# Kernel optimization log

Hardware: AMD Instinct MI355X
Metric: run time of the kernel (lower is better)

## Reference

```python
import jax, jax.numpy as jnp
import numpy as np

N = 100000   # nodes
E = 1600000  # edges
C = 64       # hidden_channels
EPS = 1e-7   # module eps
BN_EPS = 1e-5


def setup_inputs() -> dict:
    key = jax.random.key(0)
    ks = jax.random.split(key, 6)
    x = jax.random.normal(ks[0], (N, C), jnp.float32)
    edge_index = jax.random.randint(ks[1], (2, E), 0, N)
    W1 = jax.random.normal(ks[2], (2, C, 2 * C), jnp.float32) * 0.1
    b1 = jnp.zeros((2, 2 * C), jnp.float32)
    g1 = jnp.ones((2, 2 * C), jnp.float32)
    be1 = jnp.zeros((2, 2 * C), jnp.float32)
    W2 = jax.random.normal(ks[3], (2, 2 * C, C), jnp.float32) * 0.1
    b2 = jnp.zeros((2, C), jnp.float32)
    t = jnp.ones((2,), jnp.float32)       # SoftmaxAggregation learnable temperature
    scale = jnp.ones((2,), jnp.float32)   # MessageNorm learnable scale
    bn_g = jnp.ones((2, C), jnp.float32)
    bn_b = jnp.zeros((2, C), jnp.float32)
    return dict(x=x, edge_index=edge_index, t=t, scale=scale, W1=W1, b1=b1,
                g1=g1, be1=be1, W2=W2, b2=b2, bn_g=bn_g, bn_b=bn_b)


def _batchnorm(h, g, b):
    # training-mode BatchNorm1d: biased batch statistics
    mu = h.mean(axis=0)
    var = h.var(axis=0)
    return (h - mu) * jax.lax.rsqrt(var + BN_EPS) * g + b


def _gga_conv(x, src, dst, t, scale, W1, b1, g1, be1, W2, b2):
    # message: relu(x_j) + eps  (gather over source nodes)
    msg = jax.nn.relu(x[src]) + EPS                     # [E, C]
    # segment-wise (per dst node) softmax over edges, per channel
    logits = msg * t
    m = jax.ops.segment_max(logits, dst, num_segments=N)  # [N, C]
    e = jnp.exp(logits - m[dst])
    denom = jax.ops.segment_sum(e, dst, num_segments=N)   # [N, C]
    alpha = e / denom[dst]
    agg = jax.ops.segment_sum(msg * alpha, dst, num_segments=N)  # [N, C]
    # MessageNorm(learn_scale=True): x + scale * ||x|| * normalize(agg)
    msg_n = agg / jnp.maximum(jnp.linalg.norm(agg, axis=-1, keepdims=True), 1e-12)
    x_norm = jnp.linalg.norm(x, axis=-1, keepdims=True)
    out = x + msg_n * x_norm * scale
    # MLP [C, 2C, C]: Linear -> BatchNorm -> ReLU -> Linear (plain last)
    h = jax.nn.relu(_batchnorm(out @ W1 + b1, g1, be1))
    return h @ W2 + b2


def reference(x, edge_index, t, scale, W1, b1, g1, be1, W2, b2, bn_g, bn_b):
    src, dst = edge_index[0], edge_index[1]
    intter = x
    for i in range(2):  # block_size = 2
        x = _gga_conv(x, src, dst, t[i], scale[i], W1[i], b1[i], g1[i],
                      be1[i], W2[i], b2[i])
        x = _batchnorm(x, bn_g[i], bn_b[i])
        if i < 1:
            x = jax.nn.relu(x) + EPS
    # residual + relu + eps; dropout p=0 is identity
    return jax.nn.relu(intter + x) + EPS
```

## Files before the change

kernel.cpp:

```cpp
#include <hip/hip_runtime.h>
#include <hip/hip_bf16.h>

#define C 64
#define H 128
#define FEPS 1e-7f
#define BNE 1e-5f
#define BSH 9
#define BSZ 512
#define EPB 4096

typedef __attribute__((ext_vector_type(8))) short bf16x8;
typedef __attribute__((ext_vector_type(4))) float f32x4;

__device__ __forceinline__ float us2f(ushort u) {
    unsigned int x = ((unsigned int)u) << 16;
    return __uint_as_float(x);
}
__device__ __forceinline__ ushort f2us(float f) {
    __hip_bfloat16 h = __float2bfloat16(f);
    return *reinterpret_cast<ushort*>(&h);
}

__global__ __launch_bounds__(256) void bhist_k(const int* __restrict__ dst,
                                               int* __restrict__ bucket_cnt, int E, int NB) {
    __shared__ int cnt[256];
    int tid = threadIdx.x;
    cnt[tid] = 0;
    __syncthreads();
    int base = blockIdx.x * EPB;
#pragma unroll
    for (int j = 0; j < 16; j++) {
        int e = base + tid + j * 256;
        if (e < E) atomicAdd(&cnt[dst[e] >> BSH], 1);
    }
    __syncthreads();
    if (tid < NB && cnt[tid]) atomicAdd(&bucket_cnt[tid], cnt[tid]);
}

__global__ void bscan_k(const int* __restrict__ bucket_cnt, int* __restrict__ bucket_off,
                        int* __restrict__ bucket_fill, int* __restrict__ row_start,
                        int NB, int N, int E) {
    __shared__ int s[256];
    int tid = threadIdx.x;
    int v = (tid < NB) ? bucket_cnt[tid] : 0;
    s[tid] = v;
    __syncthreads();
    for (int off = 1; off < 256; off <<= 1) {
        int t = 0;
        if (tid >= off) t = s[tid - off];
        __syncthreads();
        s[tid] += t;
        __syncthreads();
    }
    int excl = s[tid] - v;
    if (tid < NB) { bucket_off[tid] = excl; bucket_fill[tid] = excl; }
    if (tid == NB - 1) bucket_off[NB] = s[tid];
    if (tid == 0) row_start[N] = E;
}

__global__ __launch_bounds__(256) void bscat_k(const int* __restrict__ src,
                                               const int* __restrict__ dst,
                                               int* __restrict__ bucket_fill,
                                               unsigned int* __restrict__ bpak, int E) {
    __shared__ int cnt[256];
    __shared__ int sbase[256];
    int tid = threadIdx.x;
    cnt[tid] = 0;
    __syncthreads();
    int base = blockIdx.x * EPB;
    int dd[16], rk[16];
#pragma unroll
    for (int j = 0; j < 16; j++) {
        int e = base + tid + j * 256;
        dd[j] = -1;
        if (e < E) {
            int d = dst[e];
            dd[j] = d;
            rk[j] = atomicAdd(&cnt[d >> BSH], 1);
        }
    }
    __syncthreads();
    if (cnt[tid]) sbase[tid] = atomicAdd(&bucket_fill[tid], cnt[tid]);
    __syncthreads();
#pragma unroll
    for (int j = 0; j < 16; j++) {
        if (dd[j] >= 0) {
            int e = base + tid + j * 256;
            int b = dd[j] >> BSH;
            int pos = sbase[b] + rk[j];
            bpak[pos] = ((unsigned int)(dd[j] & (BSZ - 1)) << 17) | (unsigned int)src[e];
        }
    }
}

__global__ __launch_bounds__(512) void bfine_k(const int* __restrict__ bucket_off,
                                               const unsigned int* __restrict__ bpak,
                                               int* __restrict__ row_start,
                                               int* __restrict__ col, int N) {
    __shared__ int cnt[BSZ];
    __shared__ int off[BSZ];
    __shared__ int fill[BSZ];
    int tid = threadIdx.x;
    int b = blockIdx.x;
    int e0 = bucket_off[b], e1 = bucket_off[b + 1];
    int nbase = b << BSH;
    cnt[tid] = 0; fill[tid] = 0;
    __syncthreads();
    for (int e = e0 + tid; e < e1; e += 512) atomicAdd(&cnt[bpak[e] >> 17], 1);
    __syncthreads();
    int v = cnt[tid];
    off[tid] = v;
    __syncthreads();
    for (int o = 1; o < 512; o <<= 1) {
        int t = 0;
        if (tid >= o) t = off[tid - o];
        __syncthreads();
        off[tid] += t;
        __syncthreads();
    }
    int excl = off[tid] - v;
    off[tid] = excl;
    __syncthreads();
    int n = nbase + tid;
    if (n < N) row_start[n] = e0 + excl;
    for (int e = e0 + tid; e < e1; e += 512) {
        unsigned int w = bpak[e];
        int loc = w >> 17;
        int r = atomicAdd(&fill[loc], 1);
        col[e0 + off[loc] + r] = (int)(w & 0x1FFFFu);
    }
}

__global__ __launch_bounds__(256) void dhist_k(const int* __restrict__ rs,
                                               int* __restrict__ dbin, int N) {
    __shared__ int h[64];
    int tid = threadIdx.x;
    if (tid < 64) h[tid] = 0;
    __syncthreads();
#pragma unroll
    for (int j = 0; j < 4; j++) {
        int i = blockIdx.x * 1024 + tid + j * 256;
        if (i < N) {
            int deg = rs[i + 1] - rs[i];
            atomicAdd(&h[min(deg, 63)], 1);
        }
    }
    __syncthreads();
    if (tid < 64 && h[tid]) atomicAdd(&dbin[tid], h[tid]);
}

__global__ void dscan_k(const int* __restrict__ dbin, int* __restrict__ dbfill) {
    __shared__ int s[64];
    int tid = threadIdx.x;
    int v = dbin[tid];
    s[tid] = v;
    __syncthreads();
    for (int o = 1; o < 64; o <<= 1) {
        int t = 0;
        if (tid >= o) t = s[tid - o];
        __syncthreads();
        s[tid] += t;
        __syncthreads();
    }
    dbfill[tid] = s[tid] - v;
}

__global__ __launch_bounds__(256) void dscat_k(const int* __restrict__ rs,
                                               int* __restrict__ dbfill,
                                               int* __restrict__ perm, int N) {
    __shared__ int cnt[64];
    __shared__ int sb[64];
    int tid = threadIdx.x;
    if (tid < 64) cnt[tid] = 0;
    __syncthreads();
    int bn[4], rk[4];
#pragma unroll
    for (int j = 0; j < 4; j++) {
        int i = blockIdx.x * 1024 + tid + j * 256;
        bn[j] = -1;
        if (i < N) {
            int deg = rs[i + 1] - rs[i];
            bn[j] = min(deg, 63);
            rk[j] = atomicAdd(&cnt[bn[j]], 1);
        }
    }
    __syncthreads();
    if (tid < 64 && cnt[tid]) sb[tid] = atomicAdd(&dbfill[tid], cnt[tid]);
    __syncthreads();
#pragma unroll
    for (int j = 0; j < 4; j++) {
        if (bn[j] >= 0) {
            int i = blockIdx.x * 1024 + tid + j * 256;
            perm[sb[bn[j]] + rk[j]] = i;
        }
    }
}

template <int AFF>
__global__ __launch_bounds__(256) void prep_k(const float* __restrict__ in,
                                              const float* __restrict__ fa,
                                              const float* __restrict__ fc,
                                              ushort* __restrict__ marr, int total4) {
    int i = blockIdx.x * 256 + threadIdx.x;
    if (i >= total4) return;
    float4 v = ((const float4*)in)[i];
    int c0 = (i * 4) & 63;
    float vv[4] = {v.x, v.y, v.z, v.w};
    ushort u[4];
#pragma unroll
    for (int j = 0; j < 4; j++) {
        float x = vv[j];
        if (AFF) {
            float xv = fmaxf(x * fa[c0 + j] + fc[c0 + j], 0.f) + FEPS;
            x = xv + FEPS;
        } else {
            x = fmaxf(x, 0.f) + FEPS;
        }
        u[j] = f2us(x);
    }
    ushort4 uv = make_ushort4(u[0], u[1], u[2], u[3]);
    ((ushort4*)marr)[i] = uv;
}

template <int MODE>
__global__ __launch_bounds__(256) void agg_k(const float* __restrict__ xin,
                                             const float* __restrict__ ta,
                                             const float* __restrict__ tc,
                                             const uint2* __restrict__ marr64,
                                             const int* __restrict__ rs,
                                             const int* __restrict__ col,
                                             const int* __restrict__ perm,
                                             const float* __restrict__ t,
                                             const float* __restrict__ sc,
                                             int layer, float* __restrict__ outb, int N) {
    int lane = threadIdx.x & 63;
    int wid = threadIdx.x >> 6;
    int q = lane >> 4;
    int ql = lane & 15;
    int gid = blockIdx.x * 16 + wid * 4 + q;
    if (gid >= N) return;
    int n = perm[gid];
    float tv = t[layer];
    float sv = sc[layer];

    int beg = rs[n], end = rs[n + 1];
    float den[4] = {0.f, 0.f, 0.f, 0.f}, num[4] = {0.f, 0.f, 0.f, 0.f};

    auto acc4 = [&](uint2 d) {
        float m0 = __uint_as_float(d.x << 16);
        float m1 = __uint_as_float(d.x & 0xffff0000u);
        float m2 = __uint_as_float(d.y << 16);
        float m3 = __uint_as_float(d.y & 0xffff0000u);
        float e0 = __expf(m0 * tv);
        float e1 = __expf(m1 * tv);
        float e2 = __expf(m2 * tv);
        float e3 = __expf(m3 * tv);
        den[0] += e0; num[0] += m0 * e0;
        den[1] += e1; num[1] += m1 * e1;
        den[2] += e2; num[2] += m2 * e2;
        den[3] += e3; num[3] += m3 * e3;
    };

    int e = beg;
    int head = (4 - (e & 3)) & 3;
    if (head > end - e) head = end - e;
    for (int i = 0; i < head; i++, e++) {
        uint2 d0 = marr64[(size_t)col[e] * 16 + ql];
        acc4(d0);
    }
    if (e + 8 <= end) {
        int4 ca = *(const int4*)(col + e);
        int4 cb = *(const int4*)(col + e + 4);
        while (true) {
            uint2 d0 = marr64[(size_t)ca.x * 16 + ql];
            uint2 d1 = marr64[(size_t)ca.y * 16 + ql];
            uint2 d2 = marr64[(size_t)ca.z * 16 + ql];
            uint2 d3 = marr64[(size_t)ca.w * 16 + ql];
            uint2 d4 = marr64[(size_t)cb.x * 16 + ql];
            uint2 d5 = marr64[(size_t)cb.y * 16 + ql];
            uint2 d6 = marr64[(size_t)cb.z * 16 + ql];
            uint2 d7 = marr64[(size_t)cb.w * 16 + ql];
            e += 8;
            bool more = (e + 8 <= end);
            if (more) {
                ca = *(const int4*)(col + e);
                cb = *(const int4*)(col + e + 4);
            }
            acc4(d0); acc4(d1); acc4(d2); acc4(d3);
            acc4(d4); acc4(d5); acc4(d6); acc4(d7);
            if (!more) break;
        }
    }
    for (; e < end; e++) {
        uint2 d0 = marr64[(size_t)col[e] * 16 + ql];
        acc4(d0);
    }

    float agg[4], aq = 0.f;
#pragma unroll
    for (int c = 0; c < 4; c++) {
        agg[c] = (den[c] > 0.f) ? (num[c] / den[c]) : 0.f;
        aq += agg[c] * agg[c];
    }

    float4 xv = ((const float4*)xin)[(size_t)n * 16 + ql];
    float xn[4];
    if (MODE == 0) {
        xn[0] = xv.x; xn[1] = xv.y; xn[2] = xv.z; xn[3] = xv.w;
    } else {
        float4 av = ((const float4*)ta)[ql];
        float4 cv = ((const float4*)tc)[ql];
        xn[0] = fmaxf(xv.x * av.x + cv.x, 0.f) + FEPS;
        xn[1] = fmaxf(xv.y * av.y + cv.y, 0.f) + FEPS;
        xn[2] = fmaxf(xv.z * av.z + cv.z, 0.f) + FEPS;
        xn[3] = fmaxf(xv.w * av.w + cv.w, 0.f) + FEPS;
    }
    float xq = xn[0] * xn[0] + xn[1] * xn[1] + xn[2] * xn[2] + xn[3] * xn[3];
    float na = aq, nx = xq;
#pragma unroll
    for (int m = 1; m <= 8; m <<= 1) {
        na += __shfl_xor(na, m, 64);
        nx += __shfl_xor(nx, m, 64);
    }
    float s = (1.0f / fmaxf(sqrtf(na), 1e-12f)) * sqrtf(nx) * sv;
    float4 o;
    o.x = xn[0] + agg[0] * s;
    o.y = xn[1] + agg[1] * s;
    o.z = xn[2] + agg[2] * s;
    o.w = xn[3] + agg[3] * s;
    ((float4*)outb)[(size_t)n * 16 + ql] = o;
}

__global__ void wprep_k(const float* __restrict__ W1, const float* __restrict__ W2,
                        ushort* __restrict__ wt1, ushort* __restrict__ wt2) {
    int idx = blockIdx.x * 256 + threadIdx.x;
    int m = idx >> 13, w = idx & 8191;
    if (m < 2) {
        int colw = w >> 6, k = w & 63;
        wt1[idx] = f2us(W1[m * 8192 + k * 128 + colw]);
    } else {
        int l = m - 2;
        int colw = w >> 7, k = w & 127;
        wt2[l * 8192 + w] = f2us(W2[l * 8192 + k * 64 + colw]);
    }
}

template <int KD, int ND, int MODE>
__global__ __launch_bounds__(256) void mlpm_k(const void* __restrict__ Ain,
                                              const float* __restrict__ fa,
                                              const float* __restrict__ fc,
                                              const ushort* __restrict__ WtT,
                                              const float* __restrict__ bias,
                                              void* __restrict__ outp,
                                              float* __restrict__ s_sum,
                                              float* __restrict__ s_ssq, int N) {
    constexpr int NT = ND / 16;
    constexpr int KS = KD / 32;
    __shared__ float ssum[ND], sssq[ND];
    int tid = threadIdx.x;
    int wave = tid >> 6, lane = tid & 63, lrow = lane & 15, kg = lane >> 4;
    if (tid < ND) { ssum[tid] = 0.f; sssq[tid] = 0.f; }
    __syncthreads();

    int base = blockIdx.x * 128;

    bf16x8 wfr[NT][KS];
#pragma unroll
    for (int t = 0; t < NT; t++)
#pragma unroll
        for (int ks = 0; ks < KS; ks++)
            wfr[t][ks] = *(const bf16x8*)(WtT + (t * 16 + lrow) * KD + ks * 32 + kg * 8);
    float bv[NT];
#pragma unroll
    for (int t = 0; t < NT; t++) bv[t] = bias[t * 16 + lrow];

    float ls[NT], lq[NT];
#pragma unroll
    for (int t = 0; t < NT; t++) { ls[t] = 0.f; lq[t] = 0.f; }

    bf16x8 afr[2][KS];
    if (MODE == 0) {
        float4 raw[2][KS][2];
#pragma unroll
        for (int rt = 0; rt < 2; rt++) {
            int arow = base + (wave * 2 + rt) * 16 + lrow;
            bool rok = arow < N;
#pragma unroll
            for (int ks = 0; ks < KS; ks++) {
                float4 z = make_float4(0.f, 0.f, 0.f, 0.f);
                raw[rt][ks][0] = z; raw[rt][ks][1] = z;
                if (rok) {
                    const float4* p = (const float4*)((const float*)Ain +
                                                      (size_t)arow * KD + ks * 32 + kg * 8);
                    raw[rt][ks][0] = p[0];
                    raw[rt][ks][1] = p[1];
                }
            }
        }
#pragma unroll
        for (int rt = 0; rt < 2; rt++)
#pragma unroll
            for (int ks = 0; ks < KS; ks++) {
                float4 v0 = raw[rt][ks][0], v1 = raw[rt][ks][1];
                bf16x8 a;
                a[0] = (short)f2us(v0.x); a[1] = (short)f2us(v0.y);
                a[2] = (short)f2us(v0.z); a[3] = (short)f2us(v0.w);
                a[4] = (short)f2us(v1.x); a[5] = (short)f2us(v1.y);
                a[6] = (short)f2us(v1.z); a[7] = (short)f2us(v1.w);
                afr[rt][ks] = a;
            }
    } else {
        uint4 raw[2][KS];
#pragma unroll
        for (int rt = 0; rt < 2; rt++) {
            int arow = base + (wave * 2 + rt) * 16 + lrow;
            bool rok = arow < N;
#pragma unroll
            for (int ks = 0; ks < KS; ks++) {
                raw[rt][ks] = make_uint4(0u, 0u, 0u, 0u);
                if (rok) raw[rt][ks] = *(const uint4*)((const ushort*)Ain +
                                                       (size_t)arow * KD + ks * 32 + kg * 8);
            }
        }
#pragma unroll
        for (int rt = 0; rt < 2; rt++)
#pragma unroll
            for (int ks = 0; ks < KS; ks++) {
                int k0 = ks * 32 + kg * 8;
                float4 a0 = *(const float4*)(fa + k0);
                float4 a1 = *(const float4*)(fa + k0 + 4);
                float4 c0 = *(const float4*)(fc + k0);
                float4 c1 = *(const float4*)(fc + k0 + 4);
                unsigned int w[4] = {raw[rt][ks].x, raw[rt][ks].y, raw[rt][ks].z, raw[rt][ks].w};
                float av[8] = {a0.x, a0.y, a0.z, a0.w, a1.x, a1.y, a1.z, a1.w};
                float cv[8] = {c0.x, c0.y, c0.z, c0.w, c1.x, c1.y, c1.z, c1.w};
                bf16x8 a;
#pragma unroll
                for (int p = 0; p < 4; p++) {
                    float f0 = us2f((ushort)(w[p] & 0xffffu));
                    float f1 = us2f((ushort)(w[p] >> 16));
                    f0 = fmaxf(f0 * av[2 * p] + cv[2 * p], 0.f);
                    f1 = fmaxf(f1 * av[2 * p + 1] + cv[2 * p + 1], 0.f);
                    a[2 * p] = (short)f2us(f0);
                    a[2 * p + 1] = (short)f2us(f1);
                }
                afr[rt][ks] = a;
            }
    }

#pragma unroll
    for (int rt = 0; rt < 2; rt++) {
        int tidx = wave * 2 + rt;
#pragma unroll
        for (int t = 0; t < NT; t++) {
            f32x4 acc = {0.f, 0.f, 0.f, 0.f};
#pragma unroll
            for (int ks = 0; ks < KS; ks++)
                acc = __builtin_amdgcn_mfma_f32_16x16x32_bf16(afr[rt][ks], wfr[t][ks], acc, 0, 0, 0);
            int colw = t * 16 + lrow;
#pragma unroll
            for (int r = 0; r < 4; r++) {
                int orow = base + tidx * 16 + kg * 4 + r;
                float v = acc[r] + bv[t];
                if (orow < N) {
                    if (MODE == 0) ((ushort*)outp)[(size_t)orow * ND + colw] = f2us(v);
                    else ((float*)outp)[(size_t)orow * ND + colw] = v;
                    ls[t] += v; lq[t] += v * v;
                }
            }
        }
    }

#pragma unroll
    for (int t = 0; t < NT; t++) {
        float a = ls[t], b = lq[t];
        a += __shfl_xor(a, 16, 64); a += __shfl_xor(a, 32, 64);
        b += __shfl_xor(b, 16, 64); b += __shfl_xor(b, 32, 64);
        if (kg == 0) {
            atomicAdd(&ssum[t * 16 + lrow], a);
            atomicAdd(&sssq[t * 16 + lrow], b);
        }
    }
    __syncthreads();
    if (tid < ND) {
        atomicAdd(&s_sum[tid], ssum[tid]);
        atomicAdd(&s_ssq[tid], sssq[tid]);
    }
}

__global__ void bnfin_k(const float* __restrict__ sum, const float* __restrict__ ssq,
                        const float* __restrict__ g, const float* __restrict__ b,
                        float* __restrict__ a, float* __restrict__ cc, int n, float invN) {
    int i = threadIdx.x;
    if (i < n) {
        float mu = sum[i] * invN;
        float var = ssq[i] * invN - mu * mu;
        float rs = rsqrtf(var + BNE);
        float gg = g[i];
        float bb = b[i];
        a[i] = rs * gg;
        cc[i] = bb - mu * rs * gg;
    }
}

__global__ void final_k(const float4* __restrict__ x0, const float4* __restrict__ y,
                        const float* __restrict__ a2, const float* __restrict__ c2,
                        float4* __restrict__ outp, int total4) {
    int i = blockIdx.x * 256 + threadIdx.x;
    if (i >= total4) return;
    int c0 = (i * 4) & 63;
    float4 yv = y[i], xv = x0[i];
    float4 o;
    o.x = fmaxf(xv.x + yv.x * a2[c0 + 0] + c2[c0 + 0], 0.f) + FEPS;
    o.y = fmaxf(xv.y + yv.y * a2[c0 + 1] + c2[c0 + 1], 0.f) + FEPS;
    o.z = fmaxf(xv.z + yv.z * a2[c0 + 2] + c2[c0 + 2], 0.f) + FEPS;
    o.w = fmaxf(xv.w + yv.w * a2[c0 + 3] + c2[c0 + 3], 0.f) + FEPS;
    outp[i] = o;
}

extern "C" void kernel_launch(void* const* d_in, const int* in_sizes, int n_in,
                              void* d_out, int out_size, void* d_ws, size_t ws_size,
                              hipStream_t stream) {
    const float* x0 = (const float*)d_in[0];
    const int* ei = (const int*)d_in[1];
    const float* t = (const float*)d_in[2];
    const float* scale = (const float*)d_in[3];
    const float* W1 = (const float*)d_in[4];
    const float* b1 = (const float*)d_in[5];
    const float* g1 = (const float*)d_in[6];
    const float* be1 = (const float*)d_in[7];
    const float* W2 = (const float*)d_in[8];
    const float* b2 = (const float*)d_in[9];
    const float* bn_g = (const float*)d_in[10];
    const float* bn_b = (const float*)d_in[11];

    const int N = in_sizes[0] / C;
    const int E = in_sizes[1] / 2;
    const int* src = ei;
    const int* dst = ei + E;
    const int NB = (N + BSZ - 1) >> BSH;

    char* ws = (char*)d_ws;
    size_t cur = 0;
    auto alloc = [&](size_t bytes) -> char* {
        char* p = ws + cur;
        cur = (cur + bytes + 255) & ~(size_t)255;
        return p;
    };
    int* bucket_cnt = (int*)alloc(256 * 4);
    float* stats = (float*)alloc(768 * 4);
    int* dbin = (int*)alloc(64 * 4);
    size_t zbytes = cur;
    float* params = (float*)alloc(768 * 4);
    int* bucket_off = (int*)alloc(257 * 4);
    int* bucket_fill = (int*)alloc(256 * 4);
    int* dbfill = (int*)alloc(64 * 4);
    int* perm = (int*)alloc((size_t)N * 4);
    int* row_start = (int*)alloc(((size_t)N + 1) * 4);
    int* col = (int*)alloc((size_t)E * 4);
    ushort* marr = (ushort*)alloc((size_t)N * C * 2);
    ushort* wt1 = (ushort*)alloc(2 * H * C * 2);
    ushort* wt2 = (ushort*)alloc(2 * C * H * 2);
    float* bout = (float*)alloc((size_t)N * C * 4);
    ushort* bh = (ushort*)alloc((size_t)N * H * 2);
    float* by = (float*)alloc((size_t)N * C * 4);
    unsigned int* bpak = (unsigned int*)bh;

    hipMemsetAsync(d_ws, 0, zbytes, stream);

    wprep_k<<<128, 256, 0, stream>>>(W1, W2, wt1, wt2);

    int nbE = (E + EPB - 1) / EPB;
    bhist_k<<<nbE, 256, 0, stream>>>(dst, bucket_cnt, E, NB);
    bscan_k<<<1, 256, 0, stream>>>(bucket_cnt, bucket_off, bucket_fill, row_start, NB, N, E);
    bscat_k<<<nbE, 256, 0, stream>>>(src, dst, bucket_fill, bpak, E);
    bfine_k<<<NB, 512, 0, stream>>>(bucket_off, bpak, row_start, col, N);

    int nbD = (N + 1023) / 1024;
    dhist_k<<<nbD, 256, 0, stream>>>(row_start, dbin, N);
    dscan_k<<<1, 64, 0, stream>>>(dbin, dbfill);
    dscat_k<<<nbD, 256, 0, stream>>>(row_start, dbfill, perm, N);

    float* sum1_0 = stats + 0;   float* ssq1_0 = stats + 128;
    float* sum2_0 = stats + 256; float* ssq2_0 = stats + 320;
    float* sum1_1 = stats + 384; float* ssq1_1 = stats + 512;
    float* sum2_1 = stats + 640; float* ssq2_1 = stats + 704;
    float* a1_0 = params + 0;   float* c1_0 = params + 128;
    float* a2_0 = params + 256; float* c2_0 = params + 320;
    float* a1_1 = params + 384; float* c1_1 = params + 512;
    float* a2_1 = params + 640; float* c2_1 = params + 704;

    const float invN = 1.0f / (float)N;
    int nbN16 = (N + 15) / 16;
    int nbT2 = (N + 127) / 128;
    int nbP = (N * C / 4 + 255) / 256;

    prep_k<0><<<nbP, 256, 0, stream>>>(x0, nullptr, nullptr, marr, N * C / 4);
    agg_k<0><<<nbN16, 256, 0, stream>>>(x0, nullptr, nullptr,
                                        (const uint2*)marr, row_start, col, perm,
                                        t, scale, 0, bout, N);
    mlpm_k<C, H, 0><<<nbT2, 256, 0, stream>>>(bout, nullptr, nullptr, wt1, b1, bh,
                                              sum1_0, ssq1_0, N);
    bnfin_k<<<1, 128, 0, stream>>>(sum1_0, ssq1_0, g1, be1, a1_0, c1_0, H, invN);
    mlpm_k<H, C, 1><<<nbT2, 256, 0, stream>>>(bh, a1_0, c1_0, wt2, b2, by,
                                              sum2_0, ssq2_0, N);
    bnfin_k<<<1, 64, 0, stream>>>(sum2_0, ssq2_0, bn_g, bn_b, a2_0, c2_0, C, invN);

    prep_k<1><<<nbP, 256, 0, stream>>>(by, a2_0, c2_0, marr, N * C / 4);
    agg_k<1><<<nbN16, 256, 0, stream>>>(by, a2_0, c2_0,
                                        (const uint2*)marr, row_start, col, perm,
                                        t, scale, 1, bout, N);
    mlpm_k<C, H, 0><<<nbT2, 256, 0, stream>>>(bout, nullptr, nullptr, wt1 + H * C, b1 + H, bh,
                                              sum1_1, ssq1_1, N);
    bnfin_k<<<1, 128, 0, stream>>>(sum1_1, ssq1_1, g1 + H, be1 + H, a1_1, c1_1, H, invN);
    mlpm_k<H, C, 1><<<nbT2, 256, 0, stream>>>(bh, a1_1, c1_1, wt2 + C * H, b2 + C, by,
                                              sum2_1, ssq2_1, N);
    bnfin_k<<<1, 64, 0, stream>>>(sum2_1, ssq2_1, bn_g + C, bn_b + C, a2_1, c2_1, C, invN);

    final_k<<<nbP, 256, 0, stream>>>((const float4*)x0, (const float4*)by, a2_1, c2_1,
                                     (float4*)d_out, N * C / 4);
}
```

Before: 345.9 us.

## Fold BN finalize into consumers and drop degree-sorted node permutation

```diff
diff --git a/kernel.cpp b/kernel.cpp
--- a/kernel.cpp
+++ b/kernel.cpp
@@ -19,6 +19,17 @@
 __device__ __forceinline__ ushort f2us(float f) {
     __hip_bfloat16 h = __float2bfloat16(f);
     return *reinterpret_cast<ushort*>(&h);
+}
+__device__ __forceinline__ void bnaff(const float* __restrict__ sum,
+                                      const float* __restrict__ ssq,
+                                      const float* __restrict__ g,
+                                      const float* __restrict__ b,
+                                      float invN, int ch, float& a, float& c) {
+    float mu = sum[ch] * invN;
+    float var = ssq[ch] * invN - mu * mu;
+    float rs = rsqrtf(var + BNE);
+    a = rs * g[ch];
+    c = b[ch] - mu * a;
 }
 
 __global__ __launch_bounds__(256) void bhist_k(const int* __restrict__ dst,
@@ -131,75 +142,13 @@
     }
 }
 
-__global__ __launch_bounds__(256) void dhist_k(const int* __restrict__ rs,
-                                               int* __restrict__ dbin, int N) {
-    __shared__ int h[64];
-    int tid = threadIdx.x;
-    if (tid < 64) h[tid] = 0;
-    __syncthreads();
-#pragma unroll
-    for (int j = 0; j < 4; j++) {
-        int i = blockIdx.x * 1024 + tid + j * 256;
-        if (i < N) {
-            int deg = rs[i + 1] - rs[i];
-            atomicAdd(&h[min(deg, 63)], 1);
-        }
-    }
-    __syncthreads();
-    if (tid < 64 && h[tid]) atomicAdd(&dbin[tid], h[tid]);
-}
-
-__global__ void dscan_k(const int* __restrict__ dbin, int* __restrict__ dbfill) {
-    __shared__ int s[64];
-    int tid = threadIdx.x;
-    int v = dbin[tid];
-    s[tid] = v;
-    __syncthreads();
-    for (int o = 1; o < 64; o <<= 1) {
-        int t = 0;
-        if (tid >= o) t = s[tid - o];
-        __syncthreads();
-        s[tid] += t;
-        __syncthreads();
-    }
-    dbfill[tid] = s[tid] - v;
-}
-
-__global__ __launch_bounds__(256) void dscat_k(const int* __restrict__ rs,
-                                               int* __restrict__ dbfill,
-                                               int* __restrict__ perm, int N) {
-    __shared__ int cnt[64];
-    __shared__ int sb[64];
-    int tid = threadIdx.x;
-    if (tid < 64) cnt[tid] = 0;
-    __syncthreads();
-    int bn[4], rk[4];
-#pragma unroll
-    for (int j = 0; j < 4; j++) {
-        int i = blockIdx.x * 1024 + tid + j * 256;
-        bn[j] = -1;
-        if (i < N) {
-            int deg = rs[i + 1] - rs[i];
-            bn[j] = min(deg, 63);
-            rk[j] = atomicAdd(&cnt[bn[j]], 1);
-        }
-    }
-    __syncthreads();
-    if (tid < 64 && cnt[tid]) sb[tid] = atomicAdd(&dbfill[tid], cnt[tid]);
-    __syncthreads();
-#pragma unroll
-    for (int j = 0; j < 4; j++) {
-        if (bn[j] >= 0) {
-            int i = blockIdx.x * 1024 + tid + j * 256;
-            perm[sb[bn[j]] + rk[j]] = i;
-        }
-    }
-}
-
 template <int AFF>
 __global__ __launch_bounds__(256) void prep_k(const float* __restrict__ in,
-                                              const float* __restrict__ fa,
-                                              const float* __restrict__ fc,
+                                              const float* __restrict__ sum,
+                                              const float* __restrict__ ssq,
+                                              const float* __restrict__ g,
+                                              const float* __restrict__ b,
+                                              float invN,
                                               ushort* __restrict__ marr, int total4) {
     int i = blockIdx.x * 256 + threadIdx.x;
     if (i >= total4) return;
@@ -211,7 +160,9 @@
     for (int j = 0; j < 4; j++) {
         float x = vv[j];
         if (AFF) {
-            float xv = fmaxf(x * fa[c0 + j] + fc[c0 + j], 0.f) + FEPS;
+            float a, cc;
+            bnaff(sum, ssq, g, b, invN, c0 + j, a, cc);
+            float xv = fmaxf(x * a + cc, 0.f) + FEPS;
             x = xv + FEPS;
         } else {
             x = fmaxf(x, 0.f) + FEPS;
@@ -224,12 +175,14 @@
 
 template <int MODE>
 __global__ __launch_bounds__(256) void agg_k(const float* __restrict__ xin,
-                                             const float* __restrict__ ta,
-                                             const float* __restrict__ tc,
+                                             const float* __restrict__ sum,
+                                             const float* __restrict__ ssq,
+                                             const float* __restrict__ g,
+                                             const float* __restrict__ b,
+                                             float invN,
                                              const uint2* __restrict__ marr64,
                                              const int* __restrict__ rs,
                                              const int* __restrict__ col,
-                                             const int* __restrict__ perm,
                                              const float* __restrict__ t,
                                              const float* __restrict__ sc,
                                              int layer, float* __restrict__ outb, int N) {
@@ -237,9 +190,8 @@
     int wid = threadIdx.x >> 6;
     int q = lane >> 4;
     int ql = lane & 15;
-    int gid = blockIdx.x * 16 + wid * 4 + q;
-    if (gid >= N) return;
-    int n = perm[gid];
+    int n = blockIdx.x * 16 + wid * 4 + q;
+    if (n >= N) return;
     float tv = t[layer];
     float sv = sc[layer];
 
@@ -308,12 +260,13 @@
     if (MODE == 0) {
         xn[0] = xv.x; xn[1] = xv.y; xn[2] = xv.z; xn[3] = xv.w;
     } else {
-        float4 av = ((const float4*)ta)[ql];
-        float4 cv = ((const float4*)tc)[ql];
-        xn[0] = fmaxf(xv.x * av.x + cv.x, 0.f) + FEPS;
-        xn[1] = fmaxf(xv.y * av.y + cv.y, 0.f) + FEPS;
-        xn[2] = fmaxf(xv.z * av.z + cv.z, 0.f) + FEPS;
-        xn[3] = fmaxf(xv.w * av.w + cv.w, 0.f) + FEPS;
+        float vv[4] = {xv.x, xv.y, xv.z, xv.w};
+#pragma unroll
+        for (int j = 0; j < 4; j++) {
+            float a, cc;
+            bnaff(sum, ssq, g, b, invN, 4 * ql + j, a, cc);
+            xn[j] = fmaxf(vv[j] * a + cc, 0.f) + FEPS;
+        }
     }
     float xq = xn[0] * xn[0] + xn[1] * xn[1] + xn[2] * xn[2] + xn[3] * xn[3];
     float na = aq, nx = xq;
@@ -347,8 +300,11 @@
 
 template <int KD, int ND, int MODE>
 __global__ __launch_bounds__(256) void mlpm_k(const void* __restrict__ Ain,
-                                              const float* __restrict__ fa,
-                                              const float* __restrict__ fc,
+                                              const float* __restrict__ sum,
+                                              const float* __restrict__ ssq,
+                                              const float* __restrict__ g,
+                                              const float* __restrict__ b,
+                                              float invN,
                                               const ushort* __restrict__ WtT,
                                               const float* __restrict__ bias,
                                               void* __restrict__ outp,
@@ -357,9 +313,17 @@
     constexpr int NT = ND / 16;
     constexpr int KS = KD / 32;
     __shared__ float ssum[ND], sssq[ND];
+    __shared__ float faf[MODE ? KD : 1][2];
     int tid = threadIdx.x;
     int wave = tid >> 6, lane = tid & 63, lrow = lane & 15, kg = lane >> 4;
     if (tid < ND) { ssum[tid] = 0.f; sssq[tid] = 0.f; }
+    if (MODE) {
+        for (int i = tid; i < KD; i += 256) {
+            float a, cc;
+            bnaff(sum, ssq, g, b, invN, i, a, cc);
+            faf[i][0] = a; faf[i][1] = cc;
+        }
+    }
     __syncthreads();
 
     int base = blockIdx.x * 128;
@@ -427,20 +391,14 @@
 #pragma unroll
             for (int ks = 0; ks < KS; ks++) {
                 int k0 = ks * 32 + kg * 8;
-                float4 a0 = *(const float4*)(fa + k0);
-                float4 a1 = *(const float4*)(fa + k0 + 4);
-                float4 c0 = *(const float4*)(fc + k0);
-                float4 c1 = *(const float4*)(fc + k0 + 4);
                 unsigned int w[4] = {raw[rt][ks].x, raw[rt][ks].y, raw[rt][ks].z, raw[rt][ks].w};
-                float av[8] = {a0.x, a0.y, a0.z, a0.w, a1.x, a1.y, a1.z, a1.w};
-                float cv[8] = {c0.x, c0.y, c0.z, c0.w, c1.x, c1.y, c1.z, c1.w};
                 bf16x8 a;
 #pragma unroll
                 for (int p = 0; p < 4; p++) {
                     float f0 = us2f((ushort)(w[p] & 0xffffu));
                     float f1 = us2f((ushort)(w[p] >> 16));
-                    f0 = fmaxf(f0 * av[2 * p] + cv[2 * p], 0.f);
-                    f1 = fmaxf(f1 * av[2 * p + 1] + cv[2 * p + 1], 0.f);
+                    f0 = fmaxf(f0 * faf[k0 + 2 * p][0] + faf[k0 + 2 * p][1], 0.f);
+                    f1 = fmaxf(f1 * faf[k0 + 2 * p + 1][0] + faf[k0 + 2 * p + 1][1], 0.f);
                     a[2 * p] = (short)f2us(f0);
                     a[2 * p + 1] = (short)f2us(f1);
                 }
@@ -473,12 +431,12 @@
 
 #pragma unroll
     for (int t = 0; t < NT; t++) {
-        float a = ls[t], b = lq[t];
+        float a = ls[t], bq = lq[t];
         a += __shfl_xor(a, 16, 64); a += __shfl_xor(a, 32, 64);
-        b += __shfl_xor(b, 16, 64); b += __shfl_xor(b, 32, 64);
+        bq += __shfl_xor(bq, 16, 64); bq += __shfl_xor(bq, 32, 64);
         if (kg == 0) {
             atomicAdd(&ssum[t * 16 + lrow], a);
-            atomicAdd(&sssq[t * 16 + lrow], b);
+            atomicAdd(&sssq[t * 16 + lrow], bq);
         }
     }
     __syncthreads();
@@ -488,33 +446,24 @@
     }
 }
 
-__global__ void bnfin_k(const float* __restrict__ sum, const float* __restrict__ ssq,
+__global__ void final_k(const float4* __restrict__ x0, const float4* __restrict__ y,
+                        const float* __restrict__ sum, const float* __restrict__ ssq,
                         const float* __restrict__ g, const float* __restrict__ b,
-                        float* __restrict__ a, float* __restrict__ cc, int n, float invN) {
-    int i = threadIdx.x;
-    if (i < n) {
-        float mu = sum[i] * invN;
-        float var = ssq[i] * invN - mu * mu;
-        float rs = rsqrtf(var + BNE);
-        float gg = g[i];
-        float bb = b[i];
-        a[i] = rs * gg;
-        cc[i] = bb - mu * rs * gg;
-    }
-}
-
-__global__ void final_k(const float4* __restrict__ x0, const float4* __restrict__ y,
-                        const float* __restrict__ a2, const float* __restrict__ c2,
-                        float4* __restrict__ outp, int total4) {
+                        float invN, float4* __restrict__ outp, int total4) {
     int i = blockIdx.x * 256 + threadIdx.x;
     if (i >= total4) return;
     int c0 = (i * 4) & 63;
     float4 yv = y[i], xv = x0[i];
-    float4 o;
-    o.x = fmaxf(xv.x + yv.x * a2[c0 + 0] + c2[c0 + 0], 0.f) + FEPS;
-    o.y = fmaxf(xv.y + yv.y * a2[c0 + 1] + c2[c0 + 1], 0.f) + FEPS;
-    o.z = fmaxf(xv.z + yv.z * a2[c0 + 2] + c2[c0 + 2], 0.f) + FEPS;
-    o.w = fmaxf(xv.w + yv.w * a2[c0 + 3] + c2[c0 + 3], 0.f) + FEPS;
+    float yy[4] = {yv.x, yv.y, yv.z, yv.w};
+    float xx[4] = {xv.x, xv.y, xv.z, xv.w};
+    float oo[4];
+#pragma unroll
+    for (int j = 0; j < 4; j++) {
+        float a, cc;
+        bnaff(sum, ssq, g, b, invN, c0 + j, a, cc);
+        oo[j] = fmaxf(xx[j] + yy[j] * a + cc, 0.f) + FEPS;
+    }
+    float4 o = make_float4(oo[0], oo[1], oo[2], oo[3]);
     outp[i] = o;
 }
 
@@ -549,13 +498,9 @@
     };
     int* bucket_cnt = (int*)alloc(256 * 4);
     float* stats = (float*)alloc(768 * 4);
-    int* dbin = (int*)alloc(64 * 4);
     size_t zbytes = cur;
-    float* params = (float*)alloc(768 * 4);
     int* bucket_off = (int*)alloc(257 * 4);
     int* bucket_fill = (int*)alloc(256 * 4);
-    int* dbfill = (int*)alloc(64 * 4);
-    int* perm = (int*)alloc((size_t)N * 4);
     int* row_start = (int*)alloc(((size_t)N + 1) * 4);
     int* col = (int*)alloc((size_t)E * 4);
     ushort* marr = (ushort*)alloc((size_t)N * C * 2);
@@ -576,47 +521,37 @@
     bscat_k<<<nbE, 256, 0, stream>>>(src, dst, bucket_fill, bpak, E);
     bfine_k<<<NB, 512, 0, stream>>>(bucket_off, bpak, row_start, col, N);
 
-    int nbD = (N + 1023) / 1024;
-    dhist_k<<<nbD, 256, 0, stream>>>(row_start, dbin, N);
-    dscan_k<<<1, 64, 0, stream>>>(dbin, dbfill);
-    dscat_k<<<nbD, 256, 0, stream>>>(row_start, dbfill, perm, N);
-
     float* sum1_0 = stats + 0;   float* ssq1_0 = stats + 128;
     float* sum2_0 = stats + 256; float* ssq2_0 = stats + 320;
     float* sum1_1 = stats + 384; float* ssq1_1 = stats + 512;
     float* sum2_1 = stats + 640; float* ssq2_1 = stats + 704;
-    float* a1_0 = params + 0;   float* c1_0 = params + 128;
-    float* a2_0 = params + 256; float* c2_0 = params + 320;
-    float* a1_1 = params + 384; float* c1_1 = params + 512;
-    float* a2_1 = params + 640; float* c2_1 = params + 704;
 
     const float invN = 1.0f / (float)N;
     int nbN16 = (N + 15) / 16;
     int nbT2 = (N + 127) / 128;
     int nbP = (N * C / 4 + 255) / 256;
 
-    prep_k<0><<<nbP, 256, 0, stream>>>(x0, nullptr, nullptr, marr, N * C / 4);
-    agg_k<0><<<nbN16, 256, 0, stream>>>(x0, nullptr, nullptr,
-                                        (const uint2*)marr, row_start, col, perm,
+    prep_k<0><<<nbP, 256, 0, stream>>>(x0, nullptr, nullptr, nullptr, nullptr, 0.f,
+                                       marr, N * C / 4);
+    agg_k<0><<<nbN16, 256, 0, stream>>>(x0, nullptr, nullptr, nullptr, nullptr, 0.f,
+                                        (const uint2*)marr, row_start, col,
                                         t, scale, 0, bout, N);
-    mlpm_k<C, H, 0><<<nbT2, 256, 0, stream>>>(bout, nullptr, nullptr, wt1, b1, bh,
-                                              sum1_0, ssq1_0, N);
-    bnfin_k<<<1, 128, 0, stream>>>(sum1_0, ssq1_0, g1, be1, a1_0, c1_0, H, invN);
-    mlpm_k<H, C, 1><<<nbT2, 256, 0, stream>>>(bh, a1_0, c1_0, wt2, b2, by,
-                                              sum2_0, ssq2_0, N);
-    bnfin_k<<<1, 64, 0, stream>>>(sum2_0, ssq2_0, bn_g, bn_b, a2_0, c2_0, C, invN);
-
-    prep_k<1><<<nbP, 256, 0, stream>>>(by, a2_0, c2_0, marr, N * C / 4);
-    agg_k<1><<<nbN16, 256, 0, stream>>>(by, a2_0, c2_0,
-                                        (const uint2*)marr, row_start, col, perm,
+    mlpm_k<C, H, 0><<<nbT2, 256, 0, stream>>>(bout, nullptr, nullptr, nullptr, nullptr, 0.f,
+                                              wt1, b1, bh, sum1_0, ssq1_0, N);
+    mlpm_k<H, C, 1><<<nbT2, 256, 0, stream>>>(bh, sum1_0, ssq1_0, g1, be1, invN,
+                                              wt2, b2, by, sum2_0, ssq2_0, N);
+
+    prep_k<1><<<nbP, 256, 0, stream>>>(by, sum2_0, ssq2_0, bn_g, bn_b, invN,
+                                       marr, N * C / 4);
+    agg_k<1><<<nbN16, 256, 0, stream>>>(by, sum2_0, ssq2_0, bn_g, bn_b, invN,
+                                        (const uint2*)marr, row_start, col,
                                         t, scale, 1, bout, N);
-    mlpm_k<C, H, 0><<<nbT2, 256, 0, stream>>>(bout, nullptr, nullptr, wt1 + H * C, b1 + H, bh,
-                                              sum1_1, ssq1_1, N);
-    bnfin_k<<<1, 128, 0, stream>>>(sum1_1, ssq1_1, g1 + H, be1 + H, a1_1, c1_1, H, invN);
-    mlpm_k<H, C, 1><<<nbT2, 256, 0, stream>>>(bh, a1_1, c1_1, wt2 + C * H, b2 + C, by,
-                                              sum2_1, ssq2_1, N);
-    bnfin_k<<<1, 64, 0, stream>>>(sum2_1, ssq2_1, bn_g + C, bn_b + C, a2_1, c2_1, C, invN);
-
-    final_k<<<nbP, 256, 0, stream>>>((const float4*)x0, (const float4*)by, a2_1, c2_1,
+    mlpm_k<C, H, 0><<<nbT2, 256, 0, stream>>>(bout, nullptr, nullptr, nullptr, nullptr, 0.f,
+                                              wt1 + H * C, b1 + H, bh, sum1_1, ssq1_1, N);
+    mlpm_k<H, C, 1><<<nbT2, 256, 0, stream>>>(bh, sum1_1, ssq1_1, g1 + H, be1 + H, invN,
+                                              wt2 + C * H, b2 + C, by, sum2_1, ssq2_1, N);
+
+    final_k<<<nbP, 256, 0, stream>>>((const float4*)x0, (const float4*)by,
+                                     sum2_1, ssq2_1, bn_g + C, bn_b + C, invN,
                                      (float4*)d_out, N * C / 4);
 }
```

New measurement: 331.0 us. -4.3%, faster.
